# Performance work log

Hardware: AMD Instinct MI355X
Metric: run time of the kernel (lower is better)

The kernel has to match this reference:

```python
import jax, jax.numpy as jnp
import numpy as np

D = 1024

def setup_inputs() -> dict:
    key = jax.random.key(0)
    k1, k2, k3, k4, k5 = jax.random.split(key, 5)
    B, S = 128, 512
    seq_output = jax.random.normal(k1, (B, S, D), dtype=jnp.float32)
    mask = jax.random.randint(k2, (B, S), 0, 2) == 1  # True = masked position
    # ensure last position is never fully-masked pathological: fine either way
    scale1 = 1.0 / np.sqrt(D)
    W1 = jax.random.normal(k3, (D, D), dtype=jnp.float32) * scale1
    b1 = jnp.zeros((D,), dtype=jnp.float32)
    w2 = jax.random.normal(k4, (D,), dtype=jnp.float32) * scale1
    return {"seq_output": seq_output, "mask": mask, "W1": W1, "b1": b1, "w2": w2}

def reference(seq_output, mask, W1, b1, w2):
    # u_last: last timestep embedding
    u_last = seq_output[:, -1, :]                           # [B, D]
    # additive attention MLP: Linear -> tanh -> Linear(D->1, no bias)
    h = jnp.tanh(jnp.einsum('bsd,de->bse', seq_output, W1) + b1)  # [B, S, D]
    scores = jnp.einsum('bsd,d->bs', h, w2)                 # [B, S]
    scores = jnp.where(mask, -1e9, scores)
    attn = jax.nn.softmax(scores, axis=-1)                  # [B, S]
    u_att = jnp.einsum('bs,bsd->bd', attn, seq_output)      # [B, D]
    return (u_last, u_att)
```

## Files before the change

### kernel.cpp

```cpp
#include <hip/hip_runtime.h>
#include <hip/hip_bf16.h>
#include <cstdint>
#include <cstddef>

#define BATCH 128
#define SEQ   512
#define DIM   1024
#define MROWS (BATCH * SEQ)

typedef short short8 __attribute__((ext_vector_type(8)));
typedef __bf16 bf16x8 __attribute__((ext_vector_type(8)));
typedef float f32x4 __attribute__((ext_vector_type(4)));

template <typename VA> struct other_frag { using type = bf16x8; };
template <> struct other_frag<bf16x8> { using type = short8; };

template <typename VA>
__device__ __forceinline__ auto try_mfma(VA a, VA b, f32x4 c, int)
    -> decltype(__builtin_amdgcn_mfma_f32_16x16x32_bf16(a, b, c, 0, 0, 0)) {
  return __builtin_amdgcn_mfma_f32_16x16x32_bf16(a, b, c, 0, 0, 0);
}
template <typename VA>
__device__ __forceinline__ f32x4 try_mfma(VA a, VA b, f32x4 c, long) {
  using O = typename other_frag<VA>::type;
  O a2 = __builtin_bit_cast(O, a);
  O b2 = __builtin_bit_cast(O, b);
  return __builtin_amdgcn_mfma_f32_16x16x32_bf16(a2, b2, c, 0, 0, 0);
}
__device__ __forceinline__ f32x4 mfma_bf16(short8 a, short8 b, f32x4 c) {
  return try_mfma(a, b, c, 0);
}

__device__ __forceinline__ unsigned short f32_to_bf16(float f) {
  union { float f; uint32_t u; } v; v.f = f;
  uint32_t u = v.u;
  u += 0x7FFFu + ((u >> 16) & 1u);
  return (unsigned short)(u >> 16);
}

__device__ __forceinline__ short8 cvt8(f32x4 a, f32x4 b) {
  bf16x8 o;
  o[0] = (__bf16)a[0]; o[1] = (__bf16)a[1]; o[2] = (__bf16)a[2]; o[3] = (__bf16)a[3];
  o[4] = (__bf16)b[0]; o[5] = (__bf16)b[1]; o[6] = (__bf16)b[2]; o[7] = (__bf16)b[3];
  return __builtin_bit_cast(short8, o);
}

__device__ __forceinline__ void gload_lds16(const void* g, void* l) {
  __builtin_amdgcn_global_load_lds(
      (__attribute__((address_space(1))) void*)g,
      (__attribute__((address_space(3))) void*)l,
      16, 0, 0);
}

__device__ __forceinline__ float fast_tanh(float x) {
  x = fminf(fmaxf(x, -15.0f), 15.0f);
  float e = __expf(2.0f * x);
  return (e - 1.0f) / (e + 1.0f);
}

__global__ __launch_bounds__(256) void w1t_kernel(const float* __restrict__ W1,
                                                  unsigned short* __restrict__ W1t) {
  __shared__ float tile[64][65];
  int bx = blockIdx.x & 15;
  int by = blockIdx.x >> 4;
  int t = threadIdx.x;
  int c = t & 63, r0 = t >> 6;
#pragma unroll
  for (int i = 0; i < 16; i++) {
    int r = i * 4 + r0;
    tile[r][c] = W1[(size_t)(by * 64 + r) * DIM + bx * 64 + c];
  }
  __syncthreads();
#pragma unroll
  for (int i = 0; i < 16; i++) {
    int r = i * 4 + r0;
    W1t[(size_t)(bx * 64 + r) * DIM + by * 64 + c] = f32_to_bf16(tile[c][r]);
  }
}

__global__ __launch_bounds__(256, 4) void gemm_score_kernel(
    const float* __restrict__ X,
    const unsigned short* __restrict__ W1t,
    const float* __restrict__ b1,
    const float* __restrict__ w2,
    float* __restrict__ scores) {
  __shared__ __align__(16) char lds[24576];

  const int tid = threadIdx.x;
  const int lane = tid & 63;
  const int w = tid >> 6;
  const int wr = w >> 1, wc = w & 1;

  const int bx = blockIdx.x;
  const int swz = (bx & 7) * 512 + (bx >> 3);
  const int m0 = (swz >> 3) * 128;
  const int n0 = (swz & 7) * 128;

  const float* aSrc[4];
#pragma unroll
  for (int i = 0; i < 4; i++) {
    int sc = i * 256 + tid;
    int row = sc >> 3;
    int j = (sc & 7) ^ (row & 7);
    aSrc[i] = X + (size_t)(m0 + row) * DIM + j * 4;
  }
  const unsigned short* bSrc[2];
#pragma unroll
  for (int i = 0; i < 2; i++) {
    int sc = i * 256 + tid;
    int srow = sc >> 3;
    int j = (sc & 7) ^ (srow & 7);
    int row = srow * 2 + (j >> 2);
    bSrc[i] = W1t + (size_t)(n0 + row) * DIM + (j & 3) * 8;
  }

  int aOffs[4][2];
#pragma unroll
  for (int mi = 0; mi < 4; mi++) {
    int row = wr * 64 + mi * 16 + (lane & 15);
#pragma unroll
    for (int c = 0; c < 2; c++) {
      int j = ((lane >> 4) * 2 + c) ^ (row & 7);
      aOffs[mi][c] = row * 128 + j * 16;
    }
  }
  int bOffs[4];
#pragma unroll
  for (int ni = 0; ni < 4; ni++) {
    int row = wc * 64 + ni * 16 + (lane & 15);
    int srow = row >> 1;
    int j = ((row & 1) * 4 + (lane >> 4)) ^ (srow & 7);
    bOffs[ni] = 16384 + srow * 128 + j * 16;
  }

  f32x4 acc[4][4];
#pragma unroll
  for (int mi = 0; mi < 4; mi++)
#pragma unroll
    for (int ni = 0; ni < 4; ni++)
      acc[mi][ni] = (f32x4){0.f, 0.f, 0.f, 0.f};

  for (int kt = 0; kt < 32; ++kt) {
    const int ko = kt * 32;
    gload_lds16(aSrc[0] + ko, lds + w * 1024);
    gload_lds16(aSrc[1] + ko, lds + 4096 + w * 1024);
    gload_lds16(aSrc[2] + ko, lds + 8192 + w * 1024);
    gload_lds16(aSrc[3] + ko, lds + 12288 + w * 1024);
    gload_lds16(bSrc[0] + ko, lds + 16384 + w * 1024);
    gload_lds16(bSrc[1] + ko, lds + 16384 + 4096 + w * 1024);
    __syncthreads();

    short8 af[4], bfv[4];
#pragma unroll
    for (int mi = 0; mi < 4; mi++) {
      f32x4 lo = *(const f32x4*)(lds + aOffs[mi][0]);
      f32x4 hi = *(const f32x4*)(lds + aOffs[mi][1]);
      af[mi] = cvt8(lo, hi);
    }
#pragma unroll
    for (int ni = 0; ni < 4; ni++)
      bfv[ni] = *(const short8*)(lds + bOffs[ni]);

    __builtin_amdgcn_s_setprio(1);
#pragma unroll
    for (int mi = 0; mi < 4; mi++)
#pragma unroll
      for (int ni = 0; ni < 4; ni++)
        acc[mi][ni] = mfma_bf16(af[mi], bfv[ni], acc[mi][ni]);
    __builtin_amdgcn_s_setprio(0);
    __syncthreads();
  }

  const int cg = lane >> 4;
  const int cl = lane & 15;
#pragma unroll
  for (int mi = 0; mi < 4; mi++) {
    float p0 = 0.f, p1 = 0.f, p2 = 0.f, p3 = 0.f;
#pragma unroll
    for (int ni = 0; ni < 4; ni++) {
      int col = n0 + wc * 64 + ni * 16 + cl;
      float w2v = w2[col];
      float b1v = b1[col];
      p0 += fast_tanh(acc[mi][ni][0] + b1v) * w2v;
      p1 += fast_tanh(acc[mi][ni][1] + b1v) * w2v;
      p2 += fast_tanh(acc[mi][ni][2] + b1v) * w2v;
      p3 += fast_tanh(acc[mi][ni][3] + b1v) * w2v;
    }
#pragma unroll
    for (int off = 1; off < 16; off <<= 1) {
      p0 += __shfl_xor(p0, off);
      p1 += __shfl_xor(p1, off);
      p2 += __shfl_xor(p2, off);
      p3 += __shfl_xor(p3, off);
    }
    if (cl == 0) {
      int row = m0 + wr * 64 + mi * 16 + cg * 4;
      atomicAdd(&scores[row + 0], p0);
      atomicAdd(&scores[row + 1], p1);
      atomicAdd(&scores[row + 2], p2);
      atomicAdd(&scores[row + 3], p3);
    }
  }
}

__global__ __launch_bounds__(256) void attn_uatt_kernel(
    const float* __restrict__ X,
    const float* __restrict__ scores,
    const int* __restrict__ mask,
    float* __restrict__ u_att,
    float* __restrict__ u_last) {
  const int b = blockIdx.x;
  const int half = blockIdx.y;
  const int tid = threadIdx.x;
  const int lane = tid & 63;
  const int wave = tid >> 6;

  __shared__ float attn[SEQ];
  __shared__ float rbuf[4];
  __shared__ float part[3][64 * 9];

  float s0 = scores[(size_t)b * SEQ + tid];
  float s1 = scores[(size_t)b * SEQ + 256 + tid];
  if (mask[(size_t)b * SEQ + tid]) s0 = -1000000000.0f;
  if (mask[(size_t)b * SEQ + 256 + tid]) s1 = -1000000000.0f;

  float mx = fmaxf(s0, s1);
#pragma unroll
  for (int off = 1; off < 64; off <<= 1) mx = fmaxf(mx, __shfl_xor(mx, off));
  if (lane == 0) rbuf[wave] = mx;
  __syncthreads();
  mx = fmaxf(fmaxf(rbuf[0], rbuf[1]), fmaxf(rbuf[2], rbuf[3]));

  float p0 = expf(s0 - mx), p1 = expf(s1 - mx);
  float sm = p0 + p1;
#pragma unroll
  for (int off = 1; off < 64; off <<= 1) sm += __shfl_xor(sm, off);
  __syncthreads();
  if (lane == 0) rbuf[wave] = sm;
  __syncthreads();
  sm = rbuf[0] + rbuf[1] + rbuf[2] + rbuf[3];
  float inv = 1.0f / sm;
  attn[tid] = p0 * inv;
  attn[tid + 256] = p1 * inv;
  __syncthreads();

  if (tid < 128) {
    ((f32x4*)u_last)[(size_t)b * 256 + half * 128 + tid] =
        ((const f32x4*)X)[((size_t)b * SEQ + (SEQ - 1)) * 256 + half * 128 + tid];
  }

  const int col = tid & 63;
  const int sh = tid >> 6;
  const f32x4* Xp = (const f32x4*)X + (size_t)b * SEQ * 256 + half * 128 + col * 2;
  f32x4 a0 = {0.f, 0.f, 0.f, 0.f}, a1 = {0.f, 0.f, 0.f, 0.f};
  for (int s = sh * 128; s < sh * 128 + 128; s++) {
    float wgt = attn[s];
    a0 += wgt * Xp[(size_t)s * 256];
    a1 += wgt * Xp[(size_t)s * 256 + 1];
  }
  if (sh) {
#pragma unroll
    for (int j = 0; j < 4; j++) part[sh - 1][col * 9 + j] = a0[j];
#pragma unroll
    for (int j = 0; j < 4; j++) part[sh - 1][col * 9 + 4 + j] = a1[j];
  }
  __syncthreads();
  if (sh == 0) {
#pragma unroll
    for (int j = 0; j < 4; j++)
      a0[j] += part[0][col * 9 + j] + part[1][col * 9 + j] + part[2][col * 9 + j];
#pragma unroll
    for (int j = 0; j < 4; j++)
      a1[j] += part[0][col * 9 + 4 + j] + part[1][col * 9 + 4 + j] + part[2][col * 9 + 4 + j];
    f32x4* dst = (f32x4*)(u_att + (size_t)b * DIM + half * 512 + col * 8);
    dst[0] = a0;
    dst[1] = a1;
  }
}

extern "C" void kernel_launch(void* const* d_in, const int* in_sizes, int n_in,
                              void* d_out, int out_size, void* d_ws, size_t ws_size,
                              hipStream_t stream) {
  const float* X    = (const float*)d_in[0];
  const int*   mask = (const int*)d_in[1];
  const float* W1   = (const float*)d_in[2];
  const float* b1   = (const float*)d_in[3];
  const float* w2   = (const float*)d_in[4];

  float* out    = (float*)d_out;
  float* u_last = out;
  float* u_att  = out + BATCH * DIM;

  char* ws = (char*)d_ws;
  unsigned short* W1t = (unsigned short*)ws;
  float* scores = (float*)(ws + (size_t)DIM * DIM * 2);

  hipMemsetAsync(scores, 0, MROWS * sizeof(float), stream);
  hipLaunchKernelGGL(w1t_kernel, dim3(256), dim3(256), 0, stream, W1, W1t);
  hipLaunchKernelGGL(gemm_score_kernel, dim3(4096), dim3(256), 0, stream,
                     X, W1t, b1, w2, scores);
  hipLaunchKernelGGL(attn_uatt_kernel, dim3(128, 2), dim3(256), 0, stream,
                     X, scores, mask, u_att, u_last);
}
```

Before: 283.1 us.

## Convert A tile to bf16 in registers before LDS and prefetch next K-slice

The fp32 A operand was previously copied straight from global into LDS with async global-to-LDS loads and converted to bf16 by each wave after reading it back. Now each thread loads its fp32 slice into registers, converts it to bf16 once, and stores it into LDS, prefetching the next K-step into registers during the current MFMA step. This halves A's LDS footprint (24KB to 16KB), removes the duplicate per-wave conversions, and halves LDS read traffic for A. The cost is extra registers and synchronous global loads in place of async direct-to-LDS transfers, which may reduce occupancy or latency hiding.

New measurement: 301.9 us. 1.07x slower.

```diff
diff --git a/kernel.cpp b/kernel.cpp
--- a/kernel.cpp
+++ b/kernel.cpp
@@ -84,7 +84,7 @@
     const float* __restrict__ b1,
     const float* __restrict__ w2,
     float* __restrict__ scores) {
-  __shared__ __align__(16) char lds[24576];
+  __shared__ __align__(16) char lds[16384];
 
   const int tid = threadIdx.x;
   const int lane = tid & 63;
@@ -96,14 +96,17 @@
   const int m0 = (swz >> 3) * 128;
   const int n0 = (swz & 7) * 128;
 
-  const float* aSrc[4];
-#pragma unroll
-  for (int i = 0; i < 4; i++) {
-    int sc = i * 256 + tid;
-    int row = sc >> 3;
-    int j = (sc & 7) ^ (row & 7);
-    aSrc[i] = X + (size_t)(m0 + row) * DIM + j * 4;
-  }
+  const f32x4* aP4 = (const f32x4*)(X + (size_t)(m0 + (tid >> 1)) * DIM) + (tid & 1) * 4;
+
+  char* aWr[2];
+  {
+    int srow = tid >> 2;
+    int j0 = ((tid >> 1) & 1) * 4 + (tid & 1) * 2;
+#pragma unroll
+    for (int c = 0; c < 2; c++)
+      aWr[c] = lds + srow * 128 + ((j0 + c) ^ (srow & 7)) * 16;
+  }
+
   const unsigned short* bSrc[2];
 #pragma unroll
   for (int i = 0; i < 2; i++) {
@@ -114,23 +117,17 @@
     bSrc[i] = W1t + (size_t)(n0 + row) * DIM + (j & 3) * 8;
   }
 
-  int aOffs[4][2];
-#pragma unroll
-  for (int mi = 0; mi < 4; mi++) {
-    int row = wr * 64 + mi * 16 + (lane & 15);
-#pragma unroll
-    for (int c = 0; c < 2; c++) {
-      int j = ((lane >> 4) * 2 + c) ^ (row & 7);
-      aOffs[mi][c] = row * 128 + j * 16;
-    }
-  }
-  int bOffs[4];
-#pragma unroll
-  for (int ni = 0; ni < 4; ni++) {
-    int row = wc * 64 + ni * 16 + (lane & 15);
-    int srow = row >> 1;
-    int j = ((row & 1) * 4 + (lane >> 4)) ^ (srow & 7);
-    bOffs[ni] = 16384 + srow * 128 + j * 16;
+  int aOffs[4], bOffs[4];
+#pragma unroll
+  for (int i = 0; i < 4; i++) {
+    int rowA = wr * 64 + i * 16 + (lane & 15);
+    int srA = rowA >> 1;
+    int jA = ((rowA & 1) * 4 + (lane >> 4)) ^ (srA & 7);
+    aOffs[i] = srA * 128 + jA * 16;
+    int rowB = wc * 64 + i * 16 + (lane & 15);
+    int srB = rowB >> 1;
+    int jB = ((rowB & 1) * 4 + (lane >> 4)) ^ (srB & 7);
+    bOffs[i] = 8192 + srB * 128 + jB * 16;
   }
 
   f32x4 acc[4][4];
@@ -140,23 +137,26 @@
     for (int ni = 0; ni < 4; ni++)
       acc[mi][ni] = (f32x4){0.f, 0.f, 0.f, 0.f};
 
+  f32x4 rc0, rc1, rc2, rc3;
+  rc0 = aP4[0]; rc1 = aP4[1]; rc2 = aP4[2]; rc3 = aP4[3];
+
   for (int kt = 0; kt < 32; ++kt) {
     const int ko = kt * 32;
-    gload_lds16(aSrc[0] + ko, lds + w * 1024);
-    gload_lds16(aSrc[1] + ko, lds + 4096 + w * 1024);
-    gload_lds16(aSrc[2] + ko, lds + 8192 + w * 1024);
-    gload_lds16(aSrc[3] + ko, lds + 12288 + w * 1024);
-    gload_lds16(bSrc[0] + ko, lds + 16384 + w * 1024);
-    gload_lds16(bSrc[1] + ko, lds + 16384 + 4096 + w * 1024);
+    gload_lds16(bSrc[0] + ko, lds + 8192 + w * 1024);
+    gload_lds16(bSrc[1] + ko, lds + 12288 + w * 1024);
+    *(short8*)aWr[0] = cvt8(rc0, rc1);
+    *(short8*)aWr[1] = cvt8(rc2, rc3);
+    f32x4 rn0, rn1, rn2, rn3;
+    if (kt + 1 < 32) {
+      const f32x4* p = aP4 + (kt + 1) * 8;
+      rn0 = p[0]; rn1 = p[1]; rn2 = p[2]; rn3 = p[3];
+    }
     __syncthreads();
 
     short8 af[4], bfv[4];
 #pragma unroll
-    for (int mi = 0; mi < 4; mi++) {
-      f32x4 lo = *(const f32x4*)(lds + aOffs[mi][0]);
-      f32x4 hi = *(const f32x4*)(lds + aOffs[mi][1]);
-      af[mi] = cvt8(lo, hi);
-    }
+    for (int mi = 0; mi < 4; mi++)
+      af[mi] = *(const short8*)(lds + aOffs[mi]);
 #pragma unroll
     for (int ni = 0; ni < 4; ni++)
       bfv[ni] = *(const short8*)(lds + bOffs[ni]);
@@ -169,6 +169,8 @@
         acc[mi][ni] = mfma_bf16(af[mi], bfv[ni], acc[mi][ni]);
     __builtin_amdgcn_s_setprio(0);
     __syncthreads();
+
+    rc0 = rn0; rc1 = rn1; rc2 = rn2; rc3 = rn3;
   }
 
   const int cg = lane >> 4;
```

## Enlarge GEMM tile to 256x256 with triple-buffered async LDS pipeline

Applied to the files above, without the earlier changes.

The score GEMM now uses 512-thread blocks computing 256x256 tiles (8 waves, each 128x64). K-tiles are loaded into a 3-stage LDS ring buffer with prefetch two stages ahead, and the loop waits on vmcnt with a single barrier per iteration instead of two syncthreads. The intent is to raise operand reuse, halve redundant X reads and hide global load latency behind MFMA work. In exchange it uses 144KB of LDS and more accumulator registers, which lowers occupancy, and the reduced barrier count means the buffer reuse ordering has to be correct.

Measured after the change: 261.7 us. 7.6% less time.

```diff
diff --git a/kernel.cpp b/kernel.cpp
--- a/kernel.cpp
+++ b/kernel.cpp
@@ -7,6 +7,7 @@
 #define SEQ   512
 #define DIM   1024
 #define MROWS (BATCH * SEQ)
+#define NT    32
 
 typedef short short8 __attribute__((ext_vector_type(8)));
 typedef __bf16 bf16x8 __attribute__((ext_vector_type(8)));
@@ -78,28 +79,28 @@
   }
 }
 
-__global__ __launch_bounds__(256, 4) void gemm_score_kernel(
+__global__ __launch_bounds__(512, 2) void gemm_score_kernel(
     const float* __restrict__ X,
     const unsigned short* __restrict__ W1t,
     const float* __restrict__ b1,
     const float* __restrict__ w2,
     float* __restrict__ scores) {
-  __shared__ __align__(16) char lds[24576];
+  __shared__ __align__(16) char lds[147456];
 
   const int tid = threadIdx.x;
   const int lane = tid & 63;
   const int w = tid >> 6;
-  const int wr = w >> 1, wc = w & 1;
+  const int wr = w >> 2, wc = w & 3;
 
   const int bx = blockIdx.x;
-  const int swz = (bx & 7) * 512 + (bx >> 3);
-  const int m0 = (swz >> 3) * 128;
-  const int n0 = (swz & 7) * 128;
+  const int swz = (bx & 7) * 128 + (bx >> 3);
+  const int m0 = (swz >> 2) * 256;
+  const int n0 = (swz & 3) * 256;
 
   const float* aSrc[4];
 #pragma unroll
   for (int i = 0; i < 4; i++) {
-    int sc = i * 256 + tid;
+    int sc = i * 512 + tid;
     int row = sc >> 3;
     int j = (sc & 7) ^ (row & 7);
     aSrc[i] = X + (size_t)(m0 + row) * DIM + j * 4;
@@ -107,74 +108,90 @@
   const unsigned short* bSrc[2];
 #pragma unroll
   for (int i = 0; i < 2; i++) {
-    int sc = i * 256 + tid;
+    int sc = i * 512 + tid;
     int srow = sc >> 3;
     int j = (sc & 7) ^ (srow & 7);
     int row = srow * 2 + (j >> 2);
     bSrc[i] = W1t + (size_t)(n0 + row) * DIM + (j & 3) * 8;
   }
 
-  int aOffs[4][2];
-#pragma unroll
-  for (int mi = 0; mi < 4; mi++) {
-    int row = wr * 64 + mi * 16 + (lane & 15);
+  int aOff[8][2];
+#pragma unroll
+  for (int mi = 0; mi < 8; mi++) {
+    int row = wr * 128 + mi * 16 + (lane & 15);
 #pragma unroll
     for (int c = 0; c < 2; c++) {
       int j = ((lane >> 4) * 2 + c) ^ (row & 7);
-      aOffs[mi][c] = row * 128 + j * 16;
+      aOff[mi][c] = row * 128 + j * 16;
     }
   }
-  int bOffs[4];
+  int bOff[4];
 #pragma unroll
   for (int ni = 0; ni < 4; ni++) {
     int row = wc * 64 + ni * 16 + (lane & 15);
     int srow = row >> 1;
-    int j = ((row & 1) * 4 + (lane >> 4)) ^ (srow & 7);
-    bOffs[ni] = 16384 + srow * 128 + j * 16;
-  }
-
-  f32x4 acc[4][4];
-#pragma unroll
-  for (int mi = 0; mi < 4; mi++)
+    int ic = ((row & 1) * 4 + (lane >> 4)) ^ (srow & 7);
+    bOff[ni] = srow * 128 + ic * 16;
+  }
+
+  f32x4 acc[8][4];
+#pragma unroll
+  for (int mi = 0; mi < 8; mi++)
 #pragma unroll
     for (int ni = 0; ni < 4; ni++)
       acc[mi][ni] = (f32x4){0.f, 0.f, 0.f, 0.f};
 
-  for (int kt = 0; kt < 32; ++kt) {
-    const int ko = kt * 32;
-    gload_lds16(aSrc[0] + ko, lds + w * 1024);
-    gload_lds16(aSrc[1] + ko, lds + 4096 + w * 1024);
-    gload_lds16(aSrc[2] + ko, lds + 8192 + w * 1024);
-    gload_lds16(aSrc[3] + ko, lds + 12288 + w * 1024);
-    gload_lds16(bSrc[0] + ko, lds + 16384 + w * 1024);
-    gload_lds16(bSrc[1] + ko, lds + 16384 + 4096 + w * 1024);
-    __syncthreads();
-
-    short8 af[4], bfv[4];
-#pragma unroll
-    for (int mi = 0; mi < 4; mi++) {
-      f32x4 lo = *(const f32x4*)(lds + aOffs[mi][0]);
-      f32x4 hi = *(const f32x4*)(lds + aOffs[mi][1]);
-      af[mi] = cvt8(lo, hi);
-    }
-#pragma unroll
-    for (int ni = 0; ni < 4; ni++)
-      bfv[ni] = *(const short8*)(lds + bOffs[ni]);
-
-    __builtin_amdgcn_s_setprio(1);
-#pragma unroll
-    for (int mi = 0; mi < 4; mi++)
-#pragma unroll
-      for (int ni = 0; ni < 4; ni++)
-        acc[mi][ni] = mfma_bf16(af[mi], bfv[ni], acc[mi][ni]);
-    __builtin_amdgcn_s_setprio(0);
-    __syncthreads();
-  }
+  short8 af[8], bfv[4];
+
+#define STAGE(S) do {                                                   \
+    const int bufA_ = ((S) % 3) * 32768;                                \
+    const int bufB_ = 98304 + ((S) % 3) * 16384;                        \
+    const int koF_ = (S) * 32;                                          \
+    gload_lds16(aSrc[0] + koF_, lds + bufA_ + w * 1024);                \
+    gload_lds16(aSrc[1] + koF_, lds + bufA_ + 8192 + w * 1024);         \
+    gload_lds16(aSrc[2] + koF_, lds + bufA_ + 16384 + w * 1024);        \
+    gload_lds16(aSrc[3] + koF_, lds + bufA_ + 24576 + w * 1024);        \
+    gload_lds16(bSrc[0] + koF_, lds + bufB_ + w * 1024);                \
+    gload_lds16(bSrc[1] + koF_, lds + bufB_ + 8192 + w * 1024);         \
+  } while (0)
+
+#define KITER(S, VMSTR) do {                                            \
+    asm volatile("s_waitcnt vmcnt(" VMSTR ")" ::: "memory");            \
+    __builtin_amdgcn_s_barrier();                                       \
+    __builtin_amdgcn_sched_barrier(0);                                  \
+    if ((S) + 2 < NT) STAGE((S) + 2);                                   \
+    const char* bufA_ = lds + ((S) % 3) * 32768;                        \
+    const char* bufB_ = lds + 98304 + ((S) % 3) * 16384;                \
+    _Pragma("unroll")                                                   \
+    for (int mi = 0; mi < 8; mi++) {                                    \
+      f32x4 lo_ = *(const f32x4*)(bufA_ + aOff[mi][0]);                 \
+      f32x4 hi_ = *(const f32x4*)(bufA_ + aOff[mi][1]);                 \
+      af[mi] = cvt8(lo_, hi_);                                          \
+    }                                                                   \
+    _Pragma("unroll")                                                   \
+    for (int ni = 0; ni < 4; ni++)                                      \
+      bfv[ni] = *(const short8*)(bufB_ + bOff[ni]);                     \
+    __builtin_amdgcn_s_setprio(1);                                      \
+    _Pragma("unroll")                                                   \
+    for (int mi = 0; mi < 8; mi++)                                      \
+      _Pragma("unroll")                                                 \
+      for (int ni = 0; ni < 4; ni++)                                    \
+        acc[mi][ni] = mfma_bf16(af[mi], bfv[ni], acc[mi][ni]);          \
+    __builtin_amdgcn_s_setprio(0);                                      \
+  } while (0)
+
+  STAGE(0); STAGE(1);
+
+  for (int s = 0; s < NT - 1; ++s) KITER(s, "6");
+  KITER(NT - 1, "0");
+
+#undef STAGE
+#undef KITER
 
   const int cg = lane >> 4;
   const int cl = lane & 15;
 #pragma unroll
-  for (int mi = 0; mi < 4; mi++) {
+  for (int mi = 0; mi < 8; mi++) {
     float p0 = 0.f, p1 = 0.f, p2 = 0.f, p3 = 0.f;
 #pragma unroll
     for (int ni = 0; ni < 4; ni++) {
@@ -194,7 +211,7 @@
       p3 += __shfl_xor(p3, off);
     }
     if (cl == 0) {
-      int row = m0 + wr * 64 + mi * 16 + cg * 4;
+      int row = m0 + wr * 128 + mi * 16 + cg * 4;
       atomicAdd(&scores[row + 0], p0);
       atomicAdd(&scores[row + 1], p1);
       atomicAdd(&scores[row + 2], p2);
@@ -297,7 +314,7 @@
 
   hipMemsetAsync(scores, 0, MROWS * sizeof(float), stream);
   hipLaunchKernelGGL(w1t_kernel, dim3(256), dim3(256), 0, stream, W1, W1t);
-  hipLaunchKernelGGL(gemm_score_kernel, dim3(4096), dim3(256), 0, stream,
+  hipLaunchKernelGGL(gemm_score_kernel, dim3(1024), dim3(512), 0, stream,
                      X, W1t, b1, w2, scores);
   hipLaunchKernelGGL(attn_uatt_kernel, dim3(128, 2), dim3(256), 0, stream,
                      X, scores, mask, u_att, u_last);
```
